# Performance work log

Measured on AMD Instinct MI355X. Metric: run time of the kernel, lower is better.

Reference implementation:

```python
import jax, jax.numpy as jnp
import numpy as np

N_TOKENS, OUT, E, H, D = 32, 1, 768, 12, 8
B, L = 64, 256
DH = E // H


def layer_norm(x, g, b, eps=1e-5):
    mu = jnp.mean(x, axis=-1, keepdims=True)
    var = jnp.mean((x - mu) ** 2, axis=-1, keepdims=True)
    return (x - mu) * jax.lax.rsqrt(var + eps) * g + b


def setup_inputs() -> dict:
    key = jax.random.key(0)
    ks = jax.random.split(key, 16)
    tokens = jax.random.randint(ks[0], (B, L), 0, N_TOKENS)
    padding = jnp.zeros((B, L), dtype=bool)
    r = jax.random.normal(ks[1], (B, L, 3), dtype=jnp.float32) * 3.0
    s = 0.02
    embed = jax.random.normal(ks[2], (N_TOKENS, E), jnp.float32) * s
    embed = embed.at[0].set(0.0)  # padding_idx=0
    inp = dict(
        tokens=tokens, padding=padding, r=r, embed=embed,
        mu=jax.random.uniform(ks[3], (D, H), jnp.float32, 0.0, 4.0),
        gamma=jax.random.uniform(ks[4], (D, H), jnp.float32, 0.1, 1.0),
        w=jax.random.normal(ks[5], (D, H), jnp.float32),
        Wqkv=jax.random.normal(ks[6], (D, E, 3 * E), jnp.float32) * s,
        bqkv=jnp.zeros((D, 3 * E), jnp.float32),
        Wo=jax.random.normal(ks[7], (D, E, E), jnp.float32) * s,
        bo=jnp.zeros((D, E), jnp.float32),
        ln1_g=jnp.ones((D, E), jnp.float32), ln1_b=jnp.zeros((D, E), jnp.float32),
        W1=jax.random.normal(ks[8], (D, E, 4 * E), jnp.float32) * s,
        b1=jnp.zeros((D, 4 * E), jnp.float32),
        W2=jax.random.normal(ks[9], (D, 4 * E, E), jnp.float32) * s,
        b2=jnp.zeros((D, E), jnp.float32),
        ln2_g=jnp.ones((D, E), jnp.float32), ln2_b=jnp.zeros((D, E), jnp.float32),
        lnf_g=jnp.ones((E,), jnp.float32), lnf_b=jnp.zeros((E,), jnp.float32),
        Wout=jax.random.normal(ks[10], (E, OUT), jnp.float32) * s,
        bout=jnp.zeros((OUT,), jnp.float32),
    )
    return inp


def reference(tokens, padding, r, embed, mu, gamma, w, Wqkv, bqkv, Wo, bo,
              ln1_g, ln1_b, W1, b1, W2, b2, ln2_g, ln2_b, lnf_g, lnf_b, Wout, bout):
    Bc, Lc = tokens.shape
    # pairwise distances (eps for grad stability at d=0 on diagonal)
    diff = r[:, :, None, :] - r[:, None, :, :]              # [B,L,L,3]
    d = jnp.sqrt(jnp.sum(diff * diff, axis=-1) + 1e-12)     # [B,L,L]
    diag = jnp.eye(Lc, dtype=bool)
    pad_pair = padding[:, None, :] | padding[:, :, None]    # [B,L,L]
    attn_mask = (pad_pair | diag)[:, None, :, :]            # [B,1,L,L] True=blocked
    pad_e = padding[:, :, None]                              # [B,L,1]
    neg = jnp.asarray(-1e9, jnp.float32)

    e = embed[tokens]                                        # [B,L,E]
    scale = 1.0 / np.sqrt(DH)
    for i in range(D):
        # learned per-head Gaussian RBF attention bias
        bias = w[i][None, :, None, None] * jnp.exp(
            -gamma[i][None, :, None, None] * (d[:, None, :, :] - mu[i][None, :, None, None]) ** 2
        )                                                    # [B,H,L,L]
        e0 = layer_norm(e, ln1_g[i], ln1_b[i])
        qkv = e0 @ Wqkv[i] + bqkv[i]
        q, k, v = jnp.split(qkv, 3, axis=-1)
        q = q.reshape(Bc, Lc, H, DH).transpose(0, 2, 1, 3)
        k = k.reshape(Bc, Lc, H, DH).transpose(0, 2, 1, 3)
        v = v.reshape(Bc, Lc, H, DH).transpose(0, 2, 1, 3)
        scores = jnp.einsum('bhid,bhjd->bhij', q, k) * scale + bias
        scores = jnp.where(attn_mask, neg, scores)
        a = jax.nn.softmax(scores, axis=-1)
        o = jnp.einsum('bhij,bhjd->bhid', a, v)
        o = o.transpose(0, 2, 1, 3).reshape(Bc, Lc, E)
        e1 = o @ Wo[i] + bo[i]
        e2 = layer_norm(e1 + e0, ln2_g[i], ln2_b[i])
        e3 = jax.nn.relu(e2 @ W1[i] + b1[i]) @ W2[i] + b2[i]
        e3 = jnp.where(pad_e, 0.0, e3)
        e = e3 + e2
    e = layer_norm(e, lnf_g, lnf_b)
    e = jnp.mean(e, axis=1)
    return e @ Wout + bout
```

## Files before the change

kernel.cpp:

```cpp
#include <hip/hip_runtime.h>
#include <cstdint>
#include <cstddef>

#define B_    64
#define L_    256
#define E_    768
#define H_    12
#define DH_   64
#define D_    8
#define FF_   3072
#define QKV3_ 2304
#define M_    (B_*L_)

typedef _Float16 f16;
typedef f16   f16x8  __attribute__((ext_vector_type(8)));
typedef float f32x4  __attribute__((ext_vector_type(4)));

__device__ __forceinline__ void gl_lds16(const void* g, void* l){
    __builtin_amdgcn_global_load_lds(
        (const __attribute__((address_space(1))) void*)g,
        (__attribute__((address_space(3))) void*)l, 16, 0, 0);
}

__global__ void sentinel_kernel(float* out, int n){
    int i = blockIdx.x*64 + threadIdx.x;
    if (i < n) out[i] = 1.0e6f;
}

__global__ __launch_bounds__(256) void gather_kernel(
    const int* __restrict__ tok, const float* __restrict__ emb, float* __restrict__ e)
{
    const int idx = blockIdx.x*256 + threadIdx.x;
    const int row = idx / E_;
    const int d   = idx - row*E_;
    e[idx] = emb[(size_t)tok[row]*E_ + d];
}

__global__ void wsplit_kernel(const float* __restrict__ W, f16* __restrict__ Hh, int K, int N)
{
    __shared__ float tile[32][33];
    const int tx = threadIdx.x, ty = threadIdx.y;
#pragma unroll
    for (int i2 = 0; i2 < 4; ++i2){
        const int k = blockIdx.y*32 + ty + i2*8;
        const int n = blockIdx.x*32 + tx;
        tile[ty + i2*8][tx] = W[(size_t)k*N + n];
    }
    __syncthreads();
    const int k2 = blockIdx.y*32 + tx;
#pragma unroll
    for (int i2 = 0; i2 < 4; ++i2){
        const int n2 = blockIdx.x*32 + ty + i2*8;
        Hh[(size_t)n2*K + k2] = (f16)tile[tx][ty + i2*8];
    }
}

__global__ __launch_bounds__(256) void ln_kernel(
    const float* __restrict__ x, const float* __restrict__ g, const float* __restrict__ bb,
    float* __restrict__ yF, f16* __restrict__ yH, f16* __restrict__ yL)
{
    __shared__ float red[256];
    const int row = blockIdx.x, tid = threadIdx.x;
    const float* xr = x + (size_t)row*E_;
    float v0 = xr[tid], v1 = xr[tid+256], v2 = xr[tid+512];
    red[tid] = v0 + v1 + v2;
    __syncthreads();
    for (int o = 128; o; o >>= 1){ if (tid < o) red[tid] += red[tid+o]; __syncthreads(); }
    const float mean = red[0] * (1.f/768.f);
    __syncthreads();
    const float d0 = v0-mean, d1 = v1-mean, d2 = v2-mean;
    red[tid] = d0*d0 + d1*d1 + d2*d2;
    __syncthreads();
    for (int o = 128; o; o >>= 1){ if (tid < o) red[tid] += red[tid+o]; __syncthreads(); }
    const float rstd = rsqrtf(red[0]*(1.f/768.f) + 1e-5f);
    const float dv[3] = {d0, d1, d2};
#pragma unroll
    for (int q = 0; q < 3; ++q){
        const int d = tid + q*256;
        const float y = dv[q]*rstd*g[d] + bb[d];
        const size_t idx = (size_t)row*E_ + d;
        if (yF) yF[idx] = y;
        if (yH){
            const f16 hi = (f16)y;
            yH[idx] = hi;
            yL[idx] = (f16)(y - (float)hi);
        }
    }
}

template<int MODE>
__global__ __launch_bounds__(256, 2) void gemm_kernel(
    const f16* __restrict__ A, const f16* __restrict__ Bh,
    const float* __restrict__ bias,
    const f16* __restrict__ exH, const f16* __restrict__ exL,
    const unsigned char* __restrict__ pad,
    float* __restrict__ Cf, f16* __restrict__ Cq,
    f16* __restrict__ qh, f16* __restrict__ kh, f16* __restrict__ vt,
    int Mn, int Nn, int Kn)
{
    __shared__ f16 sA[4][128*32];
    __shared__ f16 sB[4][128*32];
    const int tid = threadIdx.x;
    const int w = tid >> 6, l = tid & 63;
    const int nt = gridDim.x;
    const int flat = blockIdx.y * nt + blockIdx.x;
    const int xcd = flat & 7, grp = flat >> 3;
    const int bx = grp % nt;
    const int by = xcd + 8 * (grp / nt);
    const int m0 = by * 128, n0 = bx * 128;
    const int waveM = (w & 1) * 64, waveN = (w >> 1) * 64;
    const int fr = l & 15, fq = l >> 4;
    f32x4 acc[4][4] = {};

    const int e0i = tid * 8;
    const int r0  = e0i >> 5, k0o = e0i & 31;
    const int e1i = e0i + 2048;
    const int r1  = e1i >> 5, k1o = e1i & 31;

    const f16* pa0 = A  + (size_t)(m0 + r0) * Kn + k0o;
    const f16* pa1 = A  + (size_t)(m0 + r1) * Kn + k1o;
    const f16* pb0 = Bh + (size_t)(n0 + r0) * Kn + k0o;
    const f16* pb1 = Bh + (size_t)(n0 + r1) * Kn + k1o;

#define STAGE_(U, KK) do { \
        const size_t ko_ = (size_t)(KK) * 32; \
        gl_lds16(pa0 + ko_, &sA[U][e0i]); \
        gl_lds16(pa1 + ko_, &sA[U][e1i]); \
        gl_lds16(pb0 + ko_, &sB[U][e0i]); \
        gl_lds16(pb1 + ko_, &sB[U][e1i]); \
    } while(0)

#define COMPUTE_(U) do { \
        f16x8 fa[4], fb[4]; \
        _Pragma("unroll") \
        for (int i = 0; i < 4; ++i){ \
            fa[i] = *(const f16x8*)&sA[U][(waveM + i*16 + fr)*32 + fq*8]; \
            fb[i] = *(const f16x8*)&sB[U][(waveN + i*16 + fr)*32 + fq*8]; \
        } \
        __builtin_amdgcn_s_setprio(1); \
        _Pragma("unroll") \
        for (int i = 0; i < 4; ++i) \
        _Pragma("unroll") \
        for (int j = 0; j < 4; ++j) \
            acc[i][j] = __builtin_amdgcn_mfma_f32_16x16x32_f16(fa[i], fb[j], acc[i][j], 0,0,0); \
        __builtin_amdgcn_s_setprio(0); \
    } while(0)

#define WAITV12 asm volatile("s_waitcnt vmcnt(12)" ::: "memory")
#define WAITV8  asm volatile("s_waitcnt vmcnt(8)"  ::: "memory")
#define WAITV4  asm volatile("s_waitcnt vmcnt(4)"  ::: "memory")
#define WAITV0  asm volatile("s_waitcnt vmcnt(0)"  ::: "memory")
#define BAR_    do { asm volatile("" ::: "memory"); __builtin_amdgcn_s_barrier(); asm volatile("" ::: "memory"); } while(0)

    const int nsteps = Kn >> 5;
    STAGE_(0, 0);
    STAGE_(1, 1);
    STAGE_(2, 2);
    for (int s = 0; s < nsteps; s += 4){
#pragma unroll
        for (int u = 0; u < 4; ++u){
            const int st = s + u;
            if (st + 3 < nsteps){ STAGE_((u+3)&3, st+3); WAITV12; }
            else if (st + 2 < nsteps){ WAITV8; }
            else if (st + 1 < nsteps){ WAITV4; }
            else { WAITV0; }
            BAR_;
            COMPUTE_(u);
            BAR_;
        }
    }
#undef STAGE_
#undef COMPUTE_
#undef WAITV12
#undef WAITV8
#undef WAITV4
#undef WAITV0
#undef BAR_

#pragma unroll
    for (int jt = 0; jt < 4; ++jt){
        const int col = n0 + waveN + jt*16 + fr;
        const float bc = bias[col];
        int which = 0, hh = 0, dd = 0;
        if (MODE == 0){
            which = col / 768;
            const int hc = col - which*768;
            hh = hc >> 6; dd = hc & 63;
        }
#pragma unroll
        for (int it = 0; it < 4; ++it)
#pragma unroll
            for (int rg = 0; rg < 4; ++rg){
                const int row = m0 + waveM + it*16 + fq*4 + rg;
                float v = acc[it][jt][rg] + bc;
                if (MODE == 0){
                    const int bb2 = row >> 8, jj2 = row & 255;
                    const size_t bh = (size_t)bb2 * H_ + hh;
                    if (which == 0)      qh[(bh*256 + jj2)*64 + dd] = (f16)v;
                    else if (which == 1) kh[(bh*256 + jj2)*64 + dd] = (f16)v;
                    else                 vt[(bh*64 + dd)*256 + jj2] = (f16)v;
                } else {
                    const size_t idx = (size_t)row * Nn + col;
                    if (MODE == 1){
                        Cf[idx] = v + (float)exH[idx] + (float)exL[idx];
                    } else if (MODE == 2){
                        Cq[idx] = (f16)fmaxf(v, 0.f);
                    } else {
                        if (pad[row]) v = 0.f;
                        Cf[idx] = v + (float)exH[idx] + (float)exL[idx];
                    }
                }
            }
    }
}

__global__ __launch_bounds__(256, 4) void attn_kernel(
    const f16* __restrict__ qh, const f16* __restrict__ kh, const f16* __restrict__ vt,
    const float* __restrict__ rpos, const unsigned char* __restrict__ pad,
    const float* __restrict__ mu, const float* __restrict__ ga, const float* __restrict__ wv,
    f16* __restrict__ o)
{
    __shared__ f16 sK[64*72];
    __shared__ f16 sV[64*72];
    __shared__ f16 sP[4][16*72];
    __shared__ float rx[256], ry[256], rz[256], pf[256];

    const int h = blockIdx.x, b = blockIdx.y, p = blockIdx.z;
    const int tid = threadIdx.x, w = tid >> 6, l = tid & 63;
    const int fr = l & 15, fq = l >> 4;
    const float muh = mu[h], gah = ga[h], wh = wv[h];
    const size_t bh = (size_t)b * H_ + h;
    const int rowbase = b * L_;

    rx[tid] = rpos[(size_t)(rowbase+tid)*3 + 0];
    ry[tid] = rpos[(size_t)(rowbase+tid)*3 + 1];
    rz[tid] = rpos[(size_t)(rowbase+tid)*3 + 2];
    pf[tid] = pad[rowbase+tid] ? 1.f : 0.f;

    f16x8 fQ[2];
    {
        const int r = p*64 + w*16 + fr;
        const f16* qp = qh + (bh*256 + r)*64 + fq*8;
        fQ[0] = *(const f16x8*)(qp);
        fQ[1] = *(const f16x8*)(qp + 32);
    }

    float m_[4], l_[4];
    f32x4 oacc[4] = {};
#pragma unroll
    for (int rg = 0; rg < 4; ++rg){ m_[rg] = -3.0e38f; l_[rg] = 0.f; }
    __syncthreads();

    for (int c = 0; c < 4; ++c){
        __syncthreads();
        {
            const int e0 = tid*8, e1 = e0 + 2048;
            const int kr0 = e0 >> 6, kd0 = e0 & 63;
            const int kr1 = e1 >> 6, kd1 = e1 & 63;
            *(uint4*)&sK[kr0*72 + kd0] = *(const uint4*)&kh[(bh*256 + c*64 + kr0)*64 + kd0];
            *(uint4*)&sK[kr1*72 + kd1] = *(const uint4*)&kh[(bh*256 + c*64 + kr1)*64 + kd1];
            *(uint4*)&sV[kr0*72 + kd0] = *(const uint4*)&vt[(bh*64 + kr0)*256 + c*64 + kd0];
            *(uint4*)&sV[kr1*72 + kd1] = *(const uint4*)&vt[(bh*64 + kr1)*256 + c*64 + kd1];
        }
        __syncthreads();
        f32x4 sacc[4] = {};
#pragma unroll
        for (int nt = 0; nt < 4; ++nt)
#pragma unroll
            for (int kf = 0; kf < 2; ++kf){
                const f16x8 fb = *(const f16x8*)&sK[(nt*16 + fr)*72 + kf*32 + fq*8];
                sacc[nt] = __builtin_amdgcn_mfma_f32_16x16x32_f16(fQ[kf], fb, sacc[nt], 0,0,0);
            }
        float sv[4][4];
        float rmax[4] = {-3.0e38f, -3.0e38f, -3.0e38f, -3.0e38f};
        const int ibase = p*64 + w*16 + fq*4;
#pragma unroll
        for (int nt = 0; nt < 4; ++nt){
            const int j = c*64 + nt*16 + fr;
            const float jx = rx[j], jy = ry[j], jz = rz[j], jp = pf[j];
#pragma unroll
            for (int rg = 0; rg < 4; ++rg){
                const int i = ibase + rg;
                const float dx = rx[i]-jx, dy = ry[i]-jy, dz = rz[i]-jz;
                const float dist = sqrtf(dx*dx + dy*dy + dz*dz + 1e-12f);
                const float t = dist - muh;
                float s = sacc[nt][rg]*0.125f + wh*__expf(-gah*t*t);
                if ((j == i) | (pf[i] != 0.f) | (jp != 0.f)) s = -1e9f;
                sv[nt][rg] = s;
                rmax[rg] = fmaxf(rmax[rg], s);
            }
        }
#pragma unroll
        for (int rg = 0; rg < 4; ++rg){
#pragma unroll
            for (int off = 8; off >= 1; off >>= 1)
                rmax[rg] = fmaxf(rmax[rg], __shfl_xor(rmax[rg], off));
            const float mnew = fmaxf(m_[rg], rmax[rg]);
            const float alpha = __expf(m_[rg] - mnew);
            m_[rg] = mnew;
            l_[rg] *= alpha;
#pragma unroll
            for (int dt = 0; dt < 4; ++dt) oacc[dt][rg] *= alpha;
            float rs = 0.f;
#pragma unroll
            for (int nt = 0; nt < 4; ++nt){
                const float pv = __expf(sv[nt][rg] - mnew);
                sP[w][(fq*4 + rg)*72 + nt*16 + fr] = (f16)pv;
                rs += pv;
            }
#pragma unroll
            for (int off = 8; off >= 1; off >>= 1) rs += __shfl_xor(rs, off);
            l_[rg] += rs;
        }
#pragma unroll
        for (int kf = 0; kf < 2; ++kf){
            const f16x8 pa = *(const f16x8*)&sP[w][fr*72 + kf*32 + fq*8];
#pragma unroll
            for (int dt = 0; dt < 4; ++dt){
                const f16x8 vb = *(const f16x8*)&sV[(dt*16 + fr)*72 + kf*32 + fq*8];
                oacc[dt] = __builtin_amdgcn_mfma_f32_16x16x32_f16(pa, vb, oacc[dt], 0,0,0);
            }
        }
    }
    const int rglob = rowbase + p*64 + w*16 + fq*4;
#pragma unroll
    for (int rg = 0; rg < 4; ++rg){
        const float inv = 1.f / l_[rg];
#pragma unroll
        for (int dt = 0; dt < 4; ++dt)
            o[(size_t)(rglob + rg)*E_ + h*64 + dt*16 + fr] = (f16)(oacc[dt][rg]*inv);
    }
}

__global__ __launch_bounds__(256) void mean_kernel(const float* __restrict__ x, float* __restrict__ m)
{
    const int b = blockIdx.x, tid = threadIdx.x;
    const float* xb = x + (size_t)b*L_*E_;
#pragma unroll
    for (int q = 0; q < 3; ++q){
        const int d = tid + q*256;
        float s = 0.f;
        for (int l2 = 0; l2 < L_; ++l2) s += xb[(size_t)l2*E_ + d];
        m[b*E_ + d] = s * (1.f/(float)L_);
    }
}

__global__ __launch_bounds__(256) void out_kernel(
    const float* __restrict__ m, const float* __restrict__ Wout,
    const float* __restrict__ bout, float* __restrict__ out)
{
    __shared__ float red[256];
    const int b = blockIdx.x, tid = threadIdx.x;
    float s = 0.f;
#pragma unroll
    for (int q = 0; q < 3; ++q){ const int d = tid + q*256; s += m[b*E_ + d]*Wout[d]; }
    red[tid] = s;
    __syncthreads();
    for (int o = 128; o; o >>= 1){ if (tid < o) red[tid] += red[tid+o]; __syncthreads(); }
    if (tid == 0) out[b] = red[0] + bout[0];
}

extern "C" void kernel_launch(void* const* d_in, const int* in_sizes, int n_in,
                              void* d_out, int out_size, void* d_ws, size_t ws_size,
                              hipStream_t stream)
{
    const int*            tokens  = (const int*)d_in[0];
    const unsigned char*  padding = (const unsigned char*)d_in[1];
    const float*          rpos    = (const float*)d_in[2];
    const float*          embed   = (const float*)d_in[3];
    const float*          mu      = (const float*)d_in[4];
    const float*          ga      = (const float*)d_in[5];
    const float*          wv      = (const float*)d_in[6];
    const float*          Wqkv    = (const float*)d_in[7];
    const float*          bqkv    = (const float*)d_in[8];
    const float*          Wo      = (const float*)d_in[9];
    const float*          bo      = (const float*)d_in[10];
    const float*          ln1g    = (const float*)d_in[11];
    const float*          ln1b    = (const float*)d_in[12];
    const float*          W1      = (const float*)d_in[13];
    const float*          b1      = (const float*)d_in[14];
    const float*          W2      = (const float*)d_in[15];
    const float*          b2      = (const float*)d_in[16];
    const float*          ln2g    = (const float*)d_in[17];
    const float*          ln2b    = (const float*)d_in[18];
    const float*          lnfg    = (const float*)d_in[19];
    const float*          lnfb    = (const float*)d_in[20];
    const float*          Wout    = (const float*)d_in[21];
    const float*          bout    = (const float*)d_in[22];
    float* out = (float*)d_out;
    (void)in_sizes; (void)n_in;

    char* ws = (char*)d_ws;
    size_t off = 0;
    auto alloc = [&](size_t bytes)->char*{
        char* p = ws + off;
        off += (bytes + 255) & ~(size_t)255;
        return p;
    };
    const size_t PLANE = (size_t)M_*E_;
    float* e     = (float*)alloc(PLANE*4);
    char*  big   = alloc(PLANE*2*4);
    f16*   actH  = (f16*)alloc(PLANE*2);
    f16*   actL  = (f16*)alloc(PLANE*2);
    f16*   wqh   = (f16*)alloc((size_t)E_*QKV3_*2);
    f16*   woh   = (f16*)alloc((size_t)E_*E_*2);
    f16*   w1h   = (f16*)alloc((size_t)E_*FF_*2);
    f16*   w2h   = (f16*)alloc((size_t)FF_*E_*2);
    float* meanb = (float*)alloc((size_t)B_*E_*4);
    const size_t required = off;

    if (ws_size < required){
        sentinel_kernel<<<dim3((out_size+63)/64), dim3(64), 0, stream>>>(out, out_size);
        return;
    }

    f16*   qh   = (f16*)big;
    f16*   kh   = qh + PLANE;
    f16*   vt   = kh + PLANE;
    f16*   ob   = vt + PLANE;
    f16*   hbuf = (f16*)big;
    float* lnfo = (float*)big;
    float* sbuf = e;

    gather_kernel<<<dim3(M_*E_/256), dim3(256), 0, stream>>>(tokens, embed, e);

    for (int i = 0; i < D_; ++i){
        wsplit_kernel<<<dim3(QKV3_/32, E_/32), dim3(32,8), 0, stream>>>(
            Wqkv + (size_t)i*E_*QKV3_, wqh, E_, QKV3_);
        wsplit_kernel<<<dim3(E_/32, E_/32), dim3(32,8), 0, stream>>>(
            Wo + (size_t)i*E_*E_, woh, E_, E_);
        wsplit_kernel<<<dim3(FF_/32, E_/32), dim3(32,8), 0, stream>>>(
            W1 + (size_t)i*E_*FF_, w1h, E_, FF_);
        wsplit_kernel<<<dim3(E_/32, FF_/32), dim3(32,8), 0, stream>>>(
            W2 + (size_t)i*FF_*E_, w2h, FF_, E_);

        ln_kernel<<<dim3(M_), dim3(256), 0, stream>>>(e, ln1g + i*E_, ln1b + i*E_, nullptr, actH, actL);
        gemm_kernel<0><<<dim3(QKV3_/128, M_/128), dim3(256), 0, stream>>>(
            actH, wqh, bqkv + i*QKV3_, nullptr, nullptr, nullptr,
            nullptr, nullptr, qh, kh, vt, M_, QKV3_, E_);
        attn_kernel<<<dim3(H_, B_, 4), dim3(256), 0, stream>>>(
            qh, kh, vt, rpos, padding, mu + i*H_, ga + i*H_, wv + i*H_, ob);
        gemm_kernel<1><<<dim3(E_/128, M_/128), dim3(256), 0, stream>>>(
            ob, woh, bo + i*E_, actH, actL, nullptr,
            sbuf, nullptr, nullptr, nullptr, nullptr, M_, E_, E_);
        ln_kernel<<<dim3(M_), dim3(256), 0, stream>>>(sbuf, ln2g + i*E_, ln2b + i*E_, nullptr, actH, actL);
        gemm_kernel<2><<<dim3(FF_/128, M_/128), dim3(256), 0, stream>>>(
            actH, w1h, b1 + i*FF_, nullptr, nullptr, nullptr,
            nullptr, hbuf, nullptr, nullptr, nullptr, M_, FF_, E_);
        gemm_kernel<3><<<dim3(E_/128, M_/128), dim3(256), 0, stream>>>(
            hbuf, w2h, b2 + i*E_, actH, actL, padding,
            e, nullptr, nullptr, nullptr, nullptr, M_, E_, FF_);
    }

    ln_kernel<<<dim3(M_), dim3(256), 0, stream>>>(e, lnfg, lnfb, lnfo, nullptr, nullptr);
    mean_kernel<<<dim3(B_), dim3(256), 0, stream>>>(lnfo, meanb);
    out_kernel<<<dim3(B_), dim3(256), 0, stream>>>(meanb, Wout, bout, out);
}
```

Baseline: 4.720 ms.

## Enlarge GEMM tiles to 256x256 with 512 threads and XOR-swizzled LDS

The GEMM kernel moves from 128x128 tiles on 256 threads to 256x256 tiles on 512 threads. Each wave now computes a 128x64 sub-tile (8x4 MFMA accumulators), and its B fragments are reused across two halves of A. The LDS layout gains an XOR swizzle on the k-chunk to cut bank conflicts on fragment reads. This raises per-block data reuse and arithmetic intensity, at the cost of double the LDS (128 KB per block), more accumulator registers, and fewer blocks in the grid (e.g. only 192 for the N=768 GEMMs), which may hurt occupancy and load balance.

```diff
diff --git a/kernel.cpp b/kernel.cpp
--- a/kernel.cpp
+++ b/kernel.cpp
@@ -89,7 +89,7 @@
 }
 
 template<int MODE>
-__global__ __launch_bounds__(256, 2) void gemm_kernel(
+__global__ __launch_bounds__(512, 2) void gemm_kernel(
     const f16* __restrict__ A, const f16* __restrict__ Bh,
     const float* __restrict__ bias,
     const f16* __restrict__ exH, const f16* __restrict__ exL,
@@ -98,8 +98,8 @@
     f16* __restrict__ qh, f16* __restrict__ kh, f16* __restrict__ vt,
     int Mn, int Nn, int Kn)
 {
-    __shared__ f16 sA[4][128*32];
-    __shared__ f16 sB[4][128*32];
+    __shared__ f16 sA[4][256*32];
+    __shared__ f16 sB[4][256*32];
     const int tid = threadIdx.x;
     const int w = tid >> 6, l = tid & 63;
     const int nt = gridDim.x;
@@ -107,43 +107,49 @@
     const int xcd = flat & 7, grp = flat >> 3;
     const int bx = grp % nt;
     const int by = xcd + 8 * (grp / nt);
-    const int m0 = by * 128, n0 = bx * 128;
-    const int waveM = (w & 1) * 64, waveN = (w >> 1) * 64;
+    const int m0 = by * 256, n0 = bx * 256;
+    const int waveM = (w & 1) * 128, waveN = (w >> 1) * 64;
     const int fr = l & 15, fq = l >> 4;
-    f32x4 acc[4][4] = {};
-
-    const int e0i = tid * 8;
-    const int r0  = e0i >> 5, k0o = e0i & 31;
-    const int e1i = e0i + 2048;
-    const int r1  = e1i >> 5, k1o = e1i & 31;
-
-    const f16* pa0 = A  + (size_t)(m0 + r0) * Kn + k0o;
-    const f16* pa1 = A  + (size_t)(m0 + r1) * Kn + k1o;
-    const f16* pb0 = Bh + (size_t)(n0 + r0) * Kn + k0o;
-    const f16* pb1 = Bh + (size_t)(n0 + r1) * Kn + k1o;
+    const int kswz = ((fq ^ ((fr >> 1) & 3)) << 3);
+    f32x4 acc[8][4] = {};
+
+    const int rA0 = tid >> 2,  jj0 = tid & 3;
+    const int rA1 = rA0 + 128;
+    const int j0s = jj0 ^ ((rA0 >> 1) & 3);
+    const int j1s = jj0 ^ ((rA1 >> 1) & 3);
+    const f16* pa0 = A  + (size_t)(m0 + rA0) * Kn + j0s*8;
+    const f16* pa1 = A  + (size_t)(m0 + rA1) * Kn + j1s*8;
+    const f16* pb0 = Bh + (size_t)(n0 + rA0) * Kn + j0s*8;
+    const f16* pb1 = Bh + (size_t)(n0 + rA1) * Kn + j1s*8;
+    const int d0 = tid*8, d1 = tid*8 + 4096;
 
 #define STAGE_(U, KK) do { \
         const size_t ko_ = (size_t)(KK) * 32; \
-        gl_lds16(pa0 + ko_, &sA[U][e0i]); \
-        gl_lds16(pa1 + ko_, &sA[U][e1i]); \
-        gl_lds16(pb0 + ko_, &sB[U][e0i]); \
-        gl_lds16(pb1 + ko_, &sB[U][e1i]); \
+        gl_lds16(pa0 + ko_, &sA[U][d0]); \
+        gl_lds16(pa1 + ko_, &sA[U][d1]); \
+        gl_lds16(pb0 + ko_, &sB[U][d0]); \
+        gl_lds16(pb1 + ko_, &sB[U][d1]); \
     } while(0)
 
 #define COMPUTE_(U) do { \
-        f16x8 fa[4], fb[4]; \
+        f16x8 fb[4]; \
         _Pragma("unroll") \
-        for (int i = 0; i < 4; ++i){ \
-            fa[i] = *(const f16x8*)&sA[U][(waveM + i*16 + fr)*32 + fq*8]; \
-            fb[i] = *(const f16x8*)&sB[U][(waveN + i*16 + fr)*32 + fq*8]; \
+        for (int n = 0; n < 4; ++n) \
+            fb[n] = *(const f16x8*)&sB[U][(waveN + n*16 + fr)*32 + kswz]; \
+        _Pragma("unroll") \
+        for (int mh = 0; mh < 2; ++mh){ \
+            f16x8 fa[4]; \
+            _Pragma("unroll") \
+            for (int m = 0; m < 4; ++m) \
+                fa[m] = *(const f16x8*)&sA[U][(waveM + (mh*4+m)*16 + fr)*32 + kswz]; \
+            __builtin_amdgcn_s_setprio(1); \
+            _Pragma("unroll") \
+            for (int m = 0; m < 4; ++m) \
+            _Pragma("unroll") \
+            for (int n = 0; n < 4; ++n) \
+                acc[mh*4+m][n] = __builtin_amdgcn_mfma_f32_16x16x32_f16(fa[m], fb[n], acc[mh*4+m][n], 0,0,0); \
+            __builtin_amdgcn_s_setprio(0); \
         } \
-        __builtin_amdgcn_s_setprio(1); \
-        _Pragma("unroll") \
-        for (int i = 0; i < 4; ++i) \
-        _Pragma("unroll") \
-        for (int j = 0; j < 4; ++j) \
-            acc[i][j] = __builtin_amdgcn_mfma_f32_16x16x32_f16(fa[i], fb[j], acc[i][j], 0,0,0); \
-        __builtin_amdgcn_s_setprio(0); \
     } while(0)
 
 #define WAITV12 asm volatile("s_waitcnt vmcnt(12)" ::: "memory")
@@ -188,7 +194,7 @@
             hh = hc >> 6; dd = hc & 63;
         }
 #pragma unroll
-        for (int it = 0; it < 4; ++it)
+        for (int it = 0; it < 8; ++it)
 #pragma unroll
             for (int rg = 0; rg < 4; ++rg){
                 const int row = m0 + waveM + it*16 + fq*4 + rg;
@@ -435,19 +441,19 @@
             W2 + (size_t)i*FF_*E_, w2h, FF_, E_);
 
         ln_kernel<<<dim3(M_), dim3(256), 0, stream>>>(e, ln1g + i*E_, ln1b + i*E_, nullptr, actH, actL);
-        gemm_kernel<0><<<dim3(QKV3_/128, M_/128), dim3(256), 0, stream>>>(
+        gemm_kernel<0><<<dim3(QKV3_/256, M_/256), dim3(512), 0, stream>>>(
             actH, wqh, bqkv + i*QKV3_, nullptr, nullptr, nullptr,
             nullptr, nullptr, qh, kh, vt, M_, QKV3_, E_);
         attn_kernel<<<dim3(H_, B_, 4), dim3(256), 0, stream>>>(
             qh, kh, vt, rpos, padding, mu + i*H_, ga + i*H_, wv + i*H_, ob);
-        gemm_kernel<1><<<dim3(E_/128, M_/128), dim3(256), 0, stream>>>(
+        gemm_kernel<1><<<dim3(E_/256, M_/256), dim3(512), 0, stream>>>(
             ob, woh, bo + i*E_, actH, actL, nullptr,
             sbuf, nullptr, nullptr, nullptr, nullptr, M_, E_, E_);
         ln_kernel<<<dim3(M_), dim3(256), 0, stream>>>(sbuf, ln2g + i*E_, ln2b + i*E_, nullptr, actH, actL);
-        gemm_kernel<2><<<dim3(FF_/128, M_/128), dim3(256), 0, stream>>>(
+        gemm_kernel<2><<<dim3(FF_/256, M_/256), dim3(512), 0, stream>>>(
             actH, w1h, b1 + i*FF_, nullptr, nullptr, nullptr,
             nullptr, hbuf, nullptr, nullptr, nullptr, M_, FF_, E_);
-        gemm_kernel<3><<<dim3(E_/128, M_/128), dim3(256), 0, stream>>>(
+        gemm_kernel<3><<<dim3(E_/256, M_/256), dim3(512), 0, stream>>>(
             hbuf, w2h, b2 + i*E_, actH, actL, padding,
             e, nullptr, nullptr, nullptr, nullptr, M_, E_, FF_);
     }
```

After: 5.528 ms. 1.17x slower.

## Load GEMM B operand directly into registers and swizzle A in LDS

Applied to the files above, without the earlier changes.

The GEMM no longer stages the B tile through shared memory. Each wave loads its B fragments straight from global memory into double-buffered registers one k-step ahead, and only A still goes through LDS, now stored with an XOR swizzle to avoid bank conflicts. Halving the LDS footprint is paired with raising the occupancy hint to 3 blocks per SM, and the vmcnt wait thresholds are retuned for the new mix of loads. The trade-off is less coalesced global access for B, since every wave fetches its own fragments with no sharing across the block. It also adds register pressure that could spill at the higher occupancy target.

```diff
diff --git a/kernel.cpp b/kernel.cpp
--- a/kernel.cpp
+++ b/kernel.cpp
@@ -89,7 +89,7 @@
 }
 
 template<int MODE>
-__global__ __launch_bounds__(256, 2) void gemm_kernel(
+__global__ __launch_bounds__(256, 3) void gemm_kernel(
     const f16* __restrict__ A, const f16* __restrict__ Bh,
     const float* __restrict__ bias,
     const f16* __restrict__ exH, const f16* __restrict__ exL,
@@ -99,7 +99,6 @@
     int Mn, int Nn, int Kn)
 {
     __shared__ f16 sA[4][128*32];
-    __shared__ f16 sB[4][128*32];
     const int tid = threadIdx.x;
     const int w = tid >> 6, l = tid & 63;
     const int nt = gridDim.x;
@@ -110,71 +109,84 @@
     const int m0 = by * 128, n0 = bx * 128;
     const int waveM = (w & 1) * 64, waveN = (w >> 1) * 64;
     const int fr = l & 15, fq = l >> 4;
+    const int kswz = ((fq ^ ((fr >> 1) & 3)) << 3);
     f32x4 acc[4][4] = {};
 
-    const int e0i = tid * 8;
-    const int r0  = e0i >> 5, k0o = e0i & 31;
-    const int e1i = e0i + 2048;
-    const int r1  = e1i >> 5, k1o = e1i & 31;
-
-    const f16* pa0 = A  + (size_t)(m0 + r0) * Kn + k0o;
-    const f16* pa1 = A  + (size_t)(m0 + r1) * Kn + k1o;
-    const f16* pb0 = Bh + (size_t)(n0 + r0) * Kn + k0o;
-    const f16* pb1 = Bh + (size_t)(n0 + r1) * Kn + k1o;
+    const int r0 = tid >> 2, j0 = tid & 3;
+    const int r1 = r0 + 64;
+    const int j0s = j0 ^ ((r0 >> 1) & 3);
+    const int j1s = j0 ^ ((r1 >> 1) & 3);
+    const f16* pa0 = A + (size_t)(m0 + r0) * Kn + j0s*8;
+    const f16* pa1 = A + (size_t)(m0 + r1) * Kn + j1s*8;
+    const int d0 = tid*8, d1 = tid*8 + 2048;
+
+    const f16* pb[4];
+#pragma unroll
+    for (int n = 0; n < 4; ++n)
+        pb[n] = Bh + (size_t)(n0 + waveN + n*16 + fr) * Kn + fq*8;
+
+    f16x8 fbuf[2][4];
 
 #define STAGE_(U, KK) do { \
         const size_t ko_ = (size_t)(KK) * 32; \
-        gl_lds16(pa0 + ko_, &sA[U][e0i]); \
-        gl_lds16(pa1 + ko_, &sA[U][e1i]); \
-        gl_lds16(pb0 + ko_, &sB[U][e0i]); \
-        gl_lds16(pb1 + ko_, &sB[U][e1i]); \
+        gl_lds16(pa0 + ko_, &sA[U][d0]); \
+        gl_lds16(pa1 + ko_, &sA[U][d1]); \
     } while(0)
 
-#define COMPUTE_(U) do { \
-        f16x8 fa[4], fb[4]; \
+#define LOADB_(P, KK) do { \
+        const size_t ko_ = (size_t)(KK) * 32; \
         _Pragma("unroll") \
-        for (int i = 0; i < 4; ++i){ \
-            fa[i] = *(const f16x8*)&sA[U][(waveM + i*16 + fr)*32 + fq*8]; \
-            fb[i] = *(const f16x8*)&sB[U][(waveN + i*16 + fr)*32 + fq*8]; \
-        } \
+        for (int n = 0; n < 4; ++n) \
+            fbuf[P][n] = *(const f16x8*)(pb[n] + ko_); \
+    } while(0)
+
+#define COMPUTE_(U, P) do { \
+        f16x8 fa[4]; \
+        _Pragma("unroll") \
+        for (int m = 0; m < 4; ++m) \
+            fa[m] = *(const f16x8*)&sA[U][(waveM + m*16 + fr)*32 + kswz]; \
         __builtin_amdgcn_s_setprio(1); \
         _Pragma("unroll") \
-        for (int i = 0; i < 4; ++i) \
+        for (int m = 0; m < 4; ++m) \
         _Pragma("unroll") \
-        for (int j = 0; j < 4; ++j) \
-            acc[i][j] = __builtin_amdgcn_mfma_f32_16x16x32_f16(fa[i], fb[j], acc[i][j], 0,0,0); \
+        for (int n = 0; n < 4; ++n) \
+            acc[m][n] = __builtin_amdgcn_mfma_f32_16x16x32_f16(fa[m], fbuf[P][n], acc[m][n], 0,0,0); \
         __builtin_amdgcn_s_setprio(0); \
     } while(0)
 
 #define WAITV12 asm volatile("s_waitcnt vmcnt(12)" ::: "memory")
+#define WAITV10 asm volatile("s_waitcnt vmcnt(10)" ::: "memory")
 #define WAITV8  asm volatile("s_waitcnt vmcnt(8)"  ::: "memory")
 #define WAITV4  asm volatile("s_waitcnt vmcnt(4)"  ::: "memory")
-#define WAITV0  asm volatile("s_waitcnt vmcnt(0)"  ::: "memory")
 #define BAR_    do { asm volatile("" ::: "memory"); __builtin_amdgcn_s_barrier(); asm volatile("" ::: "memory"); } while(0)
 
-    const int nsteps = Kn >> 5;
+    const int ns = Kn >> 5;
     STAGE_(0, 0);
     STAGE_(1, 1);
     STAGE_(2, 2);
-    for (int s = 0; s < nsteps; s += 4){
+    LOADB_(0, 0);
+    for (int s = 0; s < ns; s += 4){
 #pragma unroll
         for (int u = 0; u < 4; ++u){
             const int st = s + u;
-            if (st + 3 < nsteps){ STAGE_((u+3)&3, st+3); WAITV12; }
-            else if (st + 2 < nsteps){ WAITV8; }
-            else if (st + 1 < nsteps){ WAITV4; }
-            else { WAITV0; }
+            if (st + 3 < ns) STAGE_((u+3)&3, st+3);
+            if (st + 1 < ns) LOADB_((u+1)&1, st+1);
+            if      (st + 3 < ns) WAITV12;
+            else if (st + 2 < ns) WAITV10;
+            else if (st + 1 < ns) WAITV8;
+            else                  WAITV4;
             BAR_;
-            COMPUTE_(u);
+            COMPUTE_(u, u&1);
             BAR_;
         }
     }
 #undef STAGE_
+#undef LOADB_
 #undef COMPUTE_
 #undef WAITV12
+#undef WAITV10
 #undef WAITV8
 #undef WAITV4
-#undef WAITV0
 #undef BAR_
 
 #pragma unroll
```

New measurement: 6.083 ms. +28.9%, slower.
